# Kernel tuning notes

Hardware: AMD Instinct MI355X
Metric: run time of the kernel (lower is better)

The kernel has to match this reference:

```python
import jax, jax.numpy as jnp
import numpy as np

D = 4096
N_HEAD = 32
KV_HEAD = 8
GS = D * KV_HEAD // N_HEAD  # 1024, kv projection width
B, S = 1, 2048


def setup_inputs() -> dict:
    key = jax.random.key(0)
    ks = jax.random.split(key, 10)
    sc = 0.02
    return {
        "x": jax.random.normal(ks[0], (B, S, D), dtype=jnp.float32),
        "y": jax.random.normal(ks[1], (B, S, D), dtype=jnp.float32),
        "Wq": jax.random.normal(ks[2], (D, D), dtype=jnp.float32) * sc,
        "bq": jax.random.normal(ks[3], (D,), dtype=jnp.float32) * sc,
        "Wk": jax.random.normal(ks[4], (D, GS), dtype=jnp.float32) * sc,
        "bk": jax.random.normal(ks[5], (GS,), dtype=jnp.float32) * sc,
        "Wv": jax.random.normal(ks[6], (D, GS), dtype=jnp.float32) * sc,
        "bv": jax.random.normal(ks[7], (GS,), dtype=jnp.float32) * sc,
        "Wo": jax.random.normal(ks[8], (D, D), dtype=jnp.float32) * sc,
        "bo": jax.random.normal(ks[9], (D,), dtype=jnp.float32) * sc,
        "n_head": N_HEAD,
        "kv_head": KV_HEAD,
    }


def reference(x, y, Wq, bq, Wk, bk, Wv, bv, Wo, bo, n_head, kv_head):
    b, s, d = x.shape
    hd = d // n_head              # per-head dim
    gvs = hd // 2                 # complex pairs per head (group_vector_size)
    q = (x @ Wq + bq).reshape(b, s, n_head, hd)
    k = (y @ Wk + bk).reshape(b, s, kv_head, hd)
    v = (y @ Wv + bv).reshape(b, s, kv_head, hd)

    # RoPE: phi = 1/5000**(i/gvs); angle[p, i] = phi[i] * p  (matrix.T in torch)
    phi = 1.0 / (5000.0 ** (jnp.arange(gvs, dtype=jnp.float32) / gvs))
    ang = jnp.arange(s, dtype=jnp.float32)[:, None] * phi[None, :]  # [S, gvs]
    cos = jnp.cos(ang)[None, :, None, :]  # [1,S,1,gvs]
    sin = jnp.sin(ang)[None, :, None, :]

    def rope(t):
        # interleaved pairs (t[...,2i], t[...,2i+1]) form complex numbers
        tr, ti = t[..., 0::2], t[..., 1::2]
        ro = tr * cos - ti * sin
        io = tr * sin + ti * cos
        return jnp.stack([ro, io], axis=-1).reshape(t.shape)

    q = rope(q)
    k = rope(k)

    # GQA: head h uses kv head h // (n_head // kv_head) -> repeat kv heads
    module = n_head // kv_head
    k = jnp.repeat(k, module, axis=2)  # [B,S,H,hd]
    v = jnp.repeat(v, module, axis=2)

    scores = jnp.einsum("bqhd,bkhd->bhqk", q, k) / jnp.sqrt(jnp.float32(hd))
    causal = jnp.tril(jnp.ones((s, s), dtype=bool))
    scores = jnp.where(causal[None, None], scores, -jnp.inf)
    attn = jax.nn.softmax(scores, axis=-1)
    out = jnp.einsum("bhqk,bkhd->bqhd", attn, v).reshape(b, s, d)
    return out @ Wo + bo
```

## Files before the change

kernel.cpp:

```cpp
#include <hip/hip_runtime.h>
#include <hip/hip_bf16.h>

typedef unsigned int uint32;
typedef unsigned short ushort16;
typedef __attribute__((ext_vector_type(8))) __bf16 bf16x8;
typedef __attribute__((ext_vector_type(4))) float f32x4;

__device__ __forceinline__ ushort16 f2bf(float f) {
    uint32 u = __float_as_uint(f);
    u += 0x7fff + ((u >> 16) & 1);
    return (ushort16)(u >> 16);
}
__device__ __forceinline__ uint32 pack2rn(float a, float b) {
    uint32 ua = __float_as_uint(a) + 0x8000u;
    uint32 ub = __float_as_uint(b) + 0x8000u;
    return __builtin_amdgcn_perm(ub, ua, 0x07060302);
}
__device__ __forceinline__ float blo(uint32 u) { return __uint_as_float(u << 16); }
__device__ __forceinline__ float bhi(uint32 u) { return __uint_as_float(u & 0xffff0000u); }

__device__ __forceinline__ void storeC(float v, float* p) { *p = v; }
__device__ __forceinline__ void storeC(float v, ushort16* p) { *p = f2bf(v); }

__device__ __forceinline__ void gload_lds16(const void* g, void* l) {
    __builtin_amdgcn_global_load_lds(
        (const __attribute__((address_space(1))) unsigned int*)g,
        (__attribute__((address_space(3))) unsigned int*)l, 16, 0, 0);
}

#define ROPE_NEGSTEP (-0.19199550593046019f)

__device__ __forceinline__ uint32 rope_pack(float tr, float ti, int ip, int s,
                                            float sc) {
    float inv = exp2f((float)ip * ROPE_NEGSTEP);
    float ang = (float)s * inv;
    float sn = __sinf(ang), cs = __cosf(ang);
    return pack2rn((tr * cs - ti * sn) * sc, (tr * sn + ti * cs) * sc);
}

__global__ __launch_bounds__(256) void prep_kernel(
    const float* __restrict__ x, const float* __restrict__ y,
    const float* __restrict__ Wq, const float* __restrict__ Wk,
    const float* __restrict__ Wv, const float* __restrict__ Wo,
    ushort16* __restrict__ xb, ushort16* __restrict__ yb,
    ushort16* __restrict__ Wqt, ushort16* __restrict__ Wkvt,
    ushort16* __restrict__ Wot)
{
    __shared__ float tile[64][65];
    const int b = blockIdx.x;
    if (b < 8192) {
        const int n8 = 1048576;
        int idx = b * 256 + threadIdx.x;
        const float* S = (idx < n8) ? x : y;
        ushort16*    D = (idx < n8) ? xb : yb;
        int i = (idx < n8) ? idx : idx - n8;
        float4 a = ((const float4*)S)[2 * i];
        float4 c = ((const float4*)S)[2 * i + 1];
        uint4 u;
        u.x = pack2rn(a.x, a.y); u.y = pack2rn(a.z, a.w);
        u.z = pack2rn(c.x, c.y); u.w = pack2rn(c.z, c.w);
        ((uint4*)D)[i] = u;
        return;
    }
    int t = b - 8192;
    int kblk = t & 63, sel = t >> 6;
    const float* W; ushort16* Wt; int N, n0;
    if (sel < 64)      { W = Wq; Wt = Wqt;  N = 4096; n0 = sel * 64; }
    else if (sel < 80) { W = Wk; Wt = Wkvt; N = 1024; n0 = (sel - 64) * 64; }
    else if (sel < 96) { W = Wv; Wt = Wkvt + (size_t)1024 * 4096; N = 1024; n0 = (sel - 80) * 64; }
    else               { W = Wo; Wt = Wot;  N = 4096; n0 = (sel - 96) * 64; }
    const int k0 = kblk * 64;
#pragma unroll
    for (int it = 0; it < 16; ++it) {
        int idx = threadIdx.x + it * 256;
        int r = idx >> 6, c = idx & 63;
        tile[r][c] = W[(size_t)(k0 + r) * N + n0 + c];
    }
    __syncthreads();
#pragma unroll
    for (int it = 0; it < 8; ++it) {
        int idx = threadIdx.x + it * 256;
        int nr = idx >> 5, kp = idx & 31;
        uint32 u = pack2rn(tile[2 * kp][nr], tile[2 * kp + 1][nr]);
        *(uint32*)&Wt[(size_t)(n0 + nr) * 4096 + k0 + 2 * kp] = u;
    }
}

__global__ __launch_bounds__(256) void gemm_qkv(
    const ushort16* __restrict__ xb, const ushort16* __restrict__ yb,
    const ushort16* __restrict__ Wqt, const ushort16* __restrict__ Wkvt,
    const float* __restrict__ bq, const float* __restrict__ bk,
    const float* __restrict__ bv, float* __restrict__ Q,
    ushort16* __restrict__ KVb)
{
    __shared__ __align__(16) ushort16 As[128 * 64];
    __shared__ __align__(16) ushort16 Bs[128 * 64];

    const bool isQ = (blockIdx.x < 32);
    const ushort16* A = isQ ? xb : yb;
    const ushort16* B = isQ ? Wqt : Wkvt;
    const int gn0 = (isQ ? (int)blockIdx.x : (int)blockIdx.x - 32) * 128;
    const int gm0 = blockIdx.y * 128;
    const int K = 4096;

    const int tid  = threadIdx.x;
    const int lane = tid & 63, wave = tid >> 6;
    const int quad = lane >> 4, m16 = lane & 15;
    const int wm = (wave >> 1) * 64, wn = (wave & 1) * 64;

    f32x4 acc[4][4];
#pragma unroll
    for (int i = 0; i < 4; ++i)
#pragma unroll
        for (int j = 0; j < 4; ++j) acc[i][j] = (f32x4){0.f, 0.f, 0.f, 0.f};

    const int rl = lane >> 3, cl = lane & 7;
    const int clog = cl ^ (rl & 7);
    const ushort16* Ag = A + (size_t)(gm0 + wave * 32 + rl) * K + clog * 8;
    const ushort16* Bg = B + (size_t)(gn0 + wave * 32 + rl) * K + clog * 8;
    char* AsW = (char*)As + wave * 4096;
    char* BsW = (char*)Bs + wave * 4096;

    for (int k0 = 0; k0 < K; k0 += 64) {
        __syncthreads();
#pragma unroll
        for (int i = 0; i < 4; ++i) {
            gload_lds16(Ag + (size_t)(8 * i) * K, AsW + i * 1024);
            gload_lds16(Bg + (size_t)(8 * i) * K, BsW + i * 1024);
        }
        Ag += 64; Bg += 64;
        __syncthreads();

#pragma unroll
        for (int s = 0; s < 2; ++s) {
            bf16x8 aF[4], bF[4];
            const int cr = s * 4 + quad;
#pragma unroll
            for (int i = 0; i < 4; ++i) {
                int r = wm + i * 16 + m16;
                aF[i] = *(const bf16x8*)&As[r * 64 + ((cr ^ (r & 7)) * 8)];
                int n = wn + i * 16 + m16;
                bF[i] = *(const bf16x8*)&Bs[n * 64 + ((cr ^ (n & 7)) * 8)];
            }
            __builtin_amdgcn_s_setprio(1);
#pragma unroll
            for (int i = 0; i < 4; ++i)
#pragma unroll
                for (int j = 0; j < 4; ++j)
                    acc[i][j] = __builtin_amdgcn_mfma_f32_16x16x32_bf16(
                        aF[i], bF[j], acc[i][j], 0, 0, 0);
            __builtin_amdgcn_s_setprio(0);
        }
    }

#pragma unroll
    for (int j = 0; j < 4; ++j) {
        int col = gn0 + wn + j * 16 + m16;
        float bb = isQ ? bq[col] : ((col < 1024) ? bk[col] : bv[col - 1024]);
#pragma unroll
        for (int i = 0; i < 4; ++i) {
            int row0 = gm0 + wm + i * 16 + quad * 4;
#pragma unroll
            for (int r = 0; r < 4; ++r) {
                float v = acc[i][j][r] + bb;
                if (isQ) Q[(size_t)(row0 + r) * 4096 + col] = v;
                else     KVb[(size_t)(row0 + r) * 2048 + col] = f2bf(v);
            }
        }
    }
}

template <typename OutT>
__global__ __launch_bounds__(256) void gemm_mfma(
    const ushort16* __restrict__ A, const ushort16* __restrict__ B,
    const float* __restrict__ b1, OutT* __restrict__ C, int N, int K)
{
    __shared__ __align__(16) ushort16 As[128 * 64];
    __shared__ __align__(16) ushort16 Bs[128 * 64];

    const int tid  = threadIdx.x;
    const int lane = tid & 63, wave = tid >> 6;
    const int quad = lane >> 4, m16 = lane & 15;
    const int wm = (wave >> 1) * 64, wn = (wave & 1) * 64;
    const int gm0 = blockIdx.y * 128, gn0 = blockIdx.x * 128;

    f32x4 acc[4][4];
#pragma unroll
    for (int i = 0; i < 4; ++i)
#pragma unroll
        for (int j = 0; j < 4; ++j) acc[i][j] = (f32x4){0.f, 0.f, 0.f, 0.f};

    const int rl = lane >> 3, cl = lane & 7;
    const int clog = cl ^ (rl & 7);
    const ushort16* Ag = A + (size_t)(gm0 + wave * 32 + rl) * K + clog * 8;
    const ushort16* Bg = B + (size_t)(gn0 + wave * 32 + rl) * K + clog * 8;
    char* AsW = (char*)As + wave * 4096;
    char* BsW = (char*)Bs + wave * 4096;

    for (int k0 = 0; k0 < K; k0 += 64) {
        __syncthreads();
#pragma unroll
        for (int i = 0; i < 4; ++i) {
            gload_lds16(Ag + (size_t)(8 * i) * K, AsW + i * 1024);
            gload_lds16(Bg + (size_t)(8 * i) * K, BsW + i * 1024);
        }
        Ag += 64; Bg += 64;
        __syncthreads();

#pragma unroll
        for (int s = 0; s < 2; ++s) {
            bf16x8 aF[4], bF[4];
            const int cr = s * 4 + quad;
#pragma unroll
            for (int i = 0; i < 4; ++i) {
                int r = wm + i * 16 + m16;
                aF[i] = *(const bf16x8*)&As[r * 64 + ((cr ^ (r & 7)) * 8)];
                int n = wn + i * 16 + m16;
                bF[i] = *(const bf16x8*)&Bs[n * 64 + ((cr ^ (n & 7)) * 8)];
            }
            __builtin_amdgcn_s_setprio(1);
#pragma unroll
            for (int i = 0; i < 4; ++i)
#pragma unroll
                for (int j = 0; j < 4; ++j)
                    acc[i][j] = __builtin_amdgcn_mfma_f32_16x16x32_bf16(
                        aF[i], bF[j], acc[i][j], 0, 0, 0);
            __builtin_amdgcn_s_setprio(0);
        }
    }

#pragma unroll
    for (int j = 0; j < 4; ++j) {
        int col = gn0 + wn + j * 16 + m16;
        float bb = b1[col];
#pragma unroll
        for (int i = 0; i < 4; ++i) {
            int row0 = gm0 + wm + i * 16 + quad * 4;
#pragma unroll
            for (int r = 0; r < 4; ++r)
                storeC(acc[i][j][r] + bb, C + (size_t)(row0 + r) * N + col);
        }
    }
}

__global__ __launch_bounds__(256) void ropek_vt_kernel(
    ushort16* __restrict__ KVb, ushort16* __restrict__ Vt)
{
    __shared__ ushort16 tile[64][66];
    const int b = blockIdx.x;
    if (b < 4096) {
        int idx = b * 256 + threadIdx.x;
        int i   = idx & 63;
        int rem = idx >> 6;
        int s   = rem >> 3, h = rem & 7;
        float inv = exp2f((float)i * ROPE_NEGSTEP);
        float ang = (float)s * inv;
        float cs = __cosf(ang), sn = __sinf(ang);
        uint32* p = (uint32*)&KVb[(size_t)s * 2048 + h * 128 + 2 * i];
        uint32 u = *p;
        float tr = blo(u), ti = bhi(u);
        *p = pack2rn(tr * cs - ti * sn, tr * sn + ti * cs);
        return;
    }
    int t = b - 4096;
    int s0 = (t >> 4) * 64, d0 = (t & 15) * 64;
#pragma unroll
    for (int it = 0; it < 2; ++it) {
        int i = threadIdx.x + it * 256;
        int r = i >> 3, c = (i & 7) * 8;
        *(uint4*)&tile[r][c] = *(const uint4*)&KVb[(size_t)(s0 + r) * 2048 + 1024 + d0 + c];
    }
    __syncthreads();
#pragma unroll
    for (int it = 0; it < 2; ++it) {
        int i = threadIdx.x + it * 256;
        int dr = i >> 3, sc = (i & 7) * 8;
        uint32 w[4];
#pragma unroll
        for (int q = 0; q < 4; ++q)
            w[q] = (uint32)tile[sc + 2 * q][dr] | ((uint32)tile[sc + 2 * q + 1][dr] << 16);
        *(uint4*)&Vt[(size_t)(d0 + dr) * 2048 + s0 + sc] = *(uint4*)w;
    }
}

__global__ __launch_bounds__(256) void flash_attn_kernel(
    const float* __restrict__ Qf, const ushort16* __restrict__ KVb,
    const ushort16* __restrict__ Vtg, ushort16* __restrict__ O)
{
    __shared__ __align__(16) ushort16 Kb[2][64 * 128];
    __shared__ __align__(16) ushort16 Vs[128 * 64];
    __shared__ __align__(16) ushort16 Ps[64 * 72];

    const int tid  = threadIdx.x;
    const int lane = tid & 63, wave = tid >> 6;
    const int quad = lane >> 4, m16 = lane & 15;
    const int h = (int)blockIdx.y, kvh = h >> 2;

    const ushort16* Kbase = KVb + kvh * 128;
    const ushort16* Vbase = Vtg + (size_t)(kvh * 128) * 2048;

    const int rK = lane >> 4;
    const ushort16* pKe = Kbase + (size_t)(wave * 16 + rK) * 2048
                        + (((lane & 15) ^ rK) * 8);
    const ushort16* pKo = Kbase + (size_t)(wave * 16 + 4 + rK) * 2048
                        + (((lane & 15) ^ (4 + rK)) * 8);
    const int rV = lane >> 3;
    const ushort16* pV  = Vbase + (size_t)(wave * 32 + rV) * 2048
                        + (((lane & 7) ^ rV) * 8);
    char* ldsK0 = (char*)&Kb[0][0] + wave * 4096;
    char* ldsK1 = (char*)&Kb[1][0] + wave * 4096;
    char* ldsV  = (char*)&Vs[0]    + wave * 4096;

#define STAGE_K(dst, kk) do {                                   \
        const ushort16* _s0 = pKe + (size_t)(kk) * 2048;        \
        const ushort16* _s1 = pKo + (size_t)(kk) * 2048;        \
        gload_lds16(_s0,            (dst));                     \
        gload_lds16(_s1,            (dst) + 1024);              \
        gload_lds16(_s0 + 8 * 2048, (dst) + 2048);              \
        gload_lds16(_s1 + 8 * 2048, (dst) + 3072);              \
    } while (0)
#define STAGE_V(kk) do {                                        \
        const ushort16* _sv = pV + (kk);                        \
        gload_lds16(_sv,             ldsV);                     \
        gload_lds16(_sv +  8 * 2048, ldsV + 1024);              \
        gload_lds16(_sv + 16 * 2048, ldsV + 2048);              \
        gload_lds16(_sv + 24 * 2048, ldsV + 3072);              \
    } while (0)

    for (int pass = 0; pass < 2; ++pass) {
        const int qi = pass ? (int)blockIdx.x : 31 - (int)blockIdx.x;
        const int q0 = qi * 64;
        const int srow = q0 + wave * 16 + m16;

        const float sc = 0.08838834764831845f * 1.4426950408889634f;
        bf16x8 qa[4];
        {
            const float* qp = Qf + (size_t)srow * 4096 + h * 128 + quad * 8;
#pragma unroll
            for (int ks = 0; ks < 4; ++ks) {
                float4 a = *(const float4*)(qp + ks * 32);
                float4 b = *(const float4*)(qp + ks * 32 + 4);
                int ip0 = quad * 4 + ks * 16;
                uint4 u;
                u.x = rope_pack(a.x, a.y, ip0 + 0, srow, sc);
                u.y = rope_pack(a.z, a.w, ip0 + 1, srow, sc);
                u.z = rope_pack(b.x, b.y, ip0 + 2, srow, sc);
                u.w = rope_pack(b.z, b.w, ip0 + 3, srow, sc);
                qa[ks] = *(bf16x8*)&u;
            }
        }

        f32x4 acc_o[8];
#pragma unroll
        for (int t = 0; t < 8; ++t) acc_o[t] = (f32x4){0.f, 0.f, 0.f, 0.f};
        float m_i[4], l_i[4];
#pragma unroll
        for (int r = 0; r < 4; ++r) { m_i[r] = -1e30f; l_i[r] = 0.f; }

        int cur = 0;
        STAGE_K(ldsK0, 0);

        for (int k0 = 0; k0 <= q0; k0 += 64) {
            __syncthreads();

            STAGE_V(k0);
            const bool pre = (k0 + 64 <= q0);
            if (pre) STAGE_K(cur ? ldsK0 : ldsK1, k0 + 64);

            const ushort16* Kcur = &Kb[cur][0];

            f32x4 sacc[4];
#pragma unroll
            for (int j = 0; j < 4; ++j) sacc[j] = (f32x4){0.f, 0.f, 0.f, 0.f};
            __builtin_amdgcn_s_setprio(1);
#pragma unroll
            for (int ks = 0; ks < 4; ++ks) {
#pragma unroll
                for (int j = 0; j < 4; ++j) {
                    int n = j * 16 + m16;
                    bf16x8 kb = *(const bf16x8*)&Kcur[n * 128 + (((ks * 4 + quad) ^ (n & 7)) * 8)];
                    sacc[j] = __builtin_amdgcn_mfma_f32_16x16x32_bf16(qa[ks], kb, sacc[j], 0, 0, 0);
                }
            }
            __builtin_amdgcn_s_setprio(0);

            if (k0 == q0) {
                int qr = wave * 16 + quad * 4;
#pragma unroll
                for (int j = 0; j < 4; ++j) {
                    int kvl = j * 16 + m16;
#pragma unroll
                    for (int r = 0; r < 4; ++r)
                        if (kvl > qr + r) sacc[j][r] = -1e30f;
                }
            }

            float rm[4];
#pragma unroll
            for (int r = 0; r < 4; ++r) {
                float v = fmaxf(fmaxf(sacc[0][r], sacc[1][r]), fmaxf(sacc[2][r], sacc[3][r]));
                v = fmaxf(v, __shfl_xor(v, 1));
                v = fmaxf(v, __shfl_xor(v, 2));
                v = fmaxf(v, __shfl_xor(v, 4));
                v = fmaxf(v, __shfl_xor(v, 8));
                rm[r] = v;
            }
            int ok = (rm[0] <= m_i[0]) & (rm[1] <= m_i[1]) &
                     (rm[2] <= m_i[2]) & (rm[3] <= m_i[3]);
            if (!__all(ok)) {
#pragma unroll
                for (int r = 0; r < 4; ++r) {
                    float mnew = fmaxf(m_i[r], rm[r]);
                    float al = exp2f(m_i[r] - mnew);
                    l_i[r] *= al;
                    m_i[r] = mnew;
#pragma unroll
                    for (int t = 0; t < 8; ++t) acc_o[t][r] *= al;
                }
            }
#pragma unroll
            for (int r = 0; r < 4; ++r) {
                float rs = 0.f;
#pragma unroll
                for (int j = 0; j < 4; ++j) {
                    float pv = exp2f(sacc[j][r] - m_i[r]);
                    sacc[j][r] = pv;
                    rs += pv;
                }
                rs += __shfl_xor(rs, 1);
                rs += __shfl_xor(rs, 2);
                rs += __shfl_xor(rs, 4);
                rs += __shfl_xor(rs, 8);
                l_i[r] += rs;
                int q = wave * 16 + quad * 4 + r;
#pragma unroll
                for (int j = 0; j < 4; ++j) {
                    int kv = j * 16 + m16;
                    Ps[q * 72 + (((kv >> 3) ^ (q & 7)) * 8) + (kv & 7)] = f2bf(sacc[j][r]);
                }
            }

            if (pre) { asm volatile("s_waitcnt vmcnt(4)" ::: "memory"); }
            else     { asm volatile("s_waitcnt vmcnt(0)" ::: "memory"); }
            __builtin_amdgcn_sched_barrier(0);
            __builtin_amdgcn_s_barrier();

            int qrow = wave * 16 + m16;
#pragma unroll
            for (int ks2 = 0; ks2 < 2; ++ks2) {
                bf16x8 pa = *(const bf16x8*)&Ps[qrow * 72 + (((ks2 * 4 + quad) ^ (qrow & 7)) * 8)];
                __builtin_amdgcn_s_setprio(1);
#pragma unroll
                for (int t = 0; t < 8; ++t) {
                    int d = t * 16 + m16;
                    bf16x8 vb = *(const bf16x8*)&Vs[d * 64 + (((ks2 * 4 + quad) ^ (d & 7)) * 8)];
                    acc_o[t] = __builtin_amdgcn_mfma_f32_16x16x32_bf16(pa, vb, acc_o[t], 0, 0, 0);
                }
                __builtin_amdgcn_s_setprio(0);
            }
            cur ^= 1;
        }

        ushort16* op = O + (size_t)(q0 + wave * 16 + quad * 4) * 4096 + h * 128 + m16;
#pragma unroll
        for (int r = 0; r < 4; ++r) {
            float inv = 1.0f / l_i[r];
#pragma unroll
            for (int t = 0; t < 8; ++t)
                op[(size_t)r * 4096 + t * 16] = f2bf(acc_o[t][r] * inv);
        }
    }
#undef STAGE_K
#undef STAGE_V
}

extern "C" void kernel_launch(void* const* d_in, const int* in_sizes, int n_in,
                              void* d_out, int out_size, void* d_ws, size_t ws_size,
                              hipStream_t stream)
{
    const float* x  = (const float*)d_in[0];
    const float* y  = (const float*)d_in[1];
    const float* Wq = (const float*)d_in[2];
    const float* bq = (const float*)d_in[3];
    const float* Wk = (const float*)d_in[4];
    const float* bk = (const float*)d_in[5];
    const float* Wv = (const float*)d_in[6];
    const float* bv = (const float*)d_in[7];
    const float* Wo = (const float*)d_in[8];
    const float* bo = (const float*)d_in[9];
    float* out = (float*)d_out;

    const size_t MB = 1024 * 1024;

    char* ws = (char*)d_ws;
    ushort16* xb   = (ushort16*)(ws);
    ushort16* yb   = (ushort16*)(ws + 16 * MB);
    ushort16* Wqt  = (ushort16*)(ws + 32 * MB);
    ushort16* Wkvt = (ushort16*)(ws + 64 * MB);
    ushort16* Wot  = (ushort16*)(ws + 80 * MB);
    ushort16* KVb  = (ushort16*)(ws + 112 * MB);
    ushort16* Vtg  = (ushort16*)(ws + 120 * MB);
    ushort16* Ao   = yb;
    float*    Q    = out;

    prep_kernel<<<18432, 256, 0, stream>>>(x, y, Wq, Wk, Wv, Wo,
                                           xb, yb, Wqt, Wkvt, Wot);

    gemm_qkv<<<dim3(48, 16), 256, 0, stream>>>(
        xb, yb, Wqt, Wkvt, bq, bk, bv, Q, KVb);

    ropek_vt_kernel<<<4608, 256, 0, stream>>>(KVb, Vtg);

    flash_attn_kernel<<<dim3(16, 32), 256, 0, stream>>>(Q, KVb, Vtg, Ao);

    gemm_mfma<float><<<dim3(32, 16), 256, 0, stream>>>(
        Ao, Wot, bo, out, 4096, 4096);
}
```

Before: 567.9 us.

## Process both causal query tiles in one KV sweep and use DPP row reductions

```diff
diff --git a/kernel.cpp b/kernel.cpp
--- a/kernel.cpp
+++ b/kernel.cpp
@@ -26,6 +26,25 @@
     __builtin_amdgcn_global_load_lds(
         (const __attribute__((address_space(1))) unsigned int*)g,
         (__attribute__((address_space(3))) unsigned int*)l, 16, 0, 0);
+}
+
+#define DPP_ROR(v, n)                                                        \
+    __uint_as_float(__builtin_amdgcn_update_dpp(                             \
+        (int)__float_as_uint(v), (int)__float_as_uint(v), 0x120 + (n),       \
+        0xf, 0xf, false))
+__device__ __forceinline__ float rowmax16(float v) {
+    v = fmaxf(v, DPP_ROR(v, 8));
+    v = fmaxf(v, DPP_ROR(v, 4));
+    v = fmaxf(v, DPP_ROR(v, 2));
+    v = fmaxf(v, DPP_ROR(v, 1));
+    return v;
+}
+__device__ __forceinline__ float rowsum16(float v) {
+    v += DPP_ROR(v, 8);
+    v += DPP_ROR(v, 4);
+    v += DPP_ROR(v, 2);
+    v += DPP_ROR(v, 1);
+    return v;
 }
 
 #define ROPE_NEGSTEP (-0.19199550593046019f)
@@ -289,7 +308,7 @@
 {
     __shared__ __align__(16) ushort16 Kb[2][64 * 128];
     __shared__ __align__(16) ushort16 Vs[128 * 64];
-    __shared__ __align__(16) ushort16 Ps[64 * 72];
+    __shared__ __align__(16) ushort16 Ps[2][64 * 72];
 
     const int tid  = threadIdx.x;
     const int lane = tid & 63, wave = tid >> 6;
@@ -327,95 +346,119 @@
         gload_lds16(_sv + 24 * 2048, ldsV + 3072);              \
     } while (0)
 
-    for (int pass = 0; pass < 2; ++pass) {
-        const int qi = pass ? (int)blockIdx.x : 31 - (int)blockIdx.x;
-        const int q0 = qi * 64;
-        const int srow = q0 + wave * 16 + m16;
-
-        const float sc = 0.08838834764831845f * 1.4426950408889634f;
-        bf16x8 qa[4];
+    const int q0A = (31 - (int)blockIdx.x) * 64;
+    const int q0B = (int)blockIdx.x * 64;
+    const float sc = 0.08838834764831845f * 1.4426950408889634f;
+
+    bf16x8 qaA[4], qaB[4];
+    {
+        const int rowA = q0A + wave * 16 + m16;
+        const int rowB = q0B + wave * 16 + m16;
+        const float* qpA = Qf + (size_t)rowA * 4096 + h * 128 + quad * 8;
+        const float* qpB = Qf + (size_t)rowB * 4096 + h * 128 + quad * 8;
+#pragma unroll
+        for (int ks = 0; ks < 4; ++ks) {
+            int ip0 = quad * 4 + ks * 16;
+            float4 a = *(const float4*)(qpA + ks * 32);
+            float4 b = *(const float4*)(qpA + ks * 32 + 4);
+            uint4 u;
+            u.x = rope_pack(a.x, a.y, ip0 + 0, rowA, sc);
+            u.y = rope_pack(a.z, a.w, ip0 + 1, rowA, sc);
+            u.z = rope_pack(b.x, b.y, ip0 + 2, rowA, sc);
+            u.w = rope_pack(b.z, b.w, ip0 + 3, rowA, sc);
+            qaA[ks] = *(bf16x8*)&u;
+            a = *(const float4*)(qpB + ks * 32);
+            b = *(const float4*)(qpB + ks * 32 + 4);
+            u.x = rope_pack(a.x, a.y, ip0 + 0, rowB, sc);
+            u.y = rope_pack(a.z, a.w, ip0 + 1, rowB, sc);
+            u.z = rope_pack(b.x, b.y, ip0 + 2, rowB, sc);
+            u.w = rope_pack(b.z, b.w, ip0 + 3, rowB, sc);
+            qaB[ks] = *(bf16x8*)&u;
+        }
+    }
+
+    f32x4 accA[8], accB[8];
+#pragma unroll
+    for (int t = 0; t < 8; ++t) {
+        accA[t] = (f32x4){0.f, 0.f, 0.f, 0.f};
+        accB[t] = (f32x4){0.f, 0.f, 0.f, 0.f};
+    }
+    float mA[4], lA[4], mB[4], lB[4];
+#pragma unroll
+    for (int r = 0; r < 4; ++r) {
+        mA[r] = -1e30f; lA[r] = 0.f; mB[r] = -1e30f; lB[r] = 0.f;
+    }
+
+    int cur = 0;
+    STAGE_K(ldsK0, 0);
+
+    for (int k0 = 0; k0 <= q0A; k0 += 64) {
+        __syncthreads();
+
+        STAGE_V(k0);
+        const bool pre = (k0 + 64 <= q0A);
+        if (pre) STAGE_K(cur ? ldsK0 : ldsK1, k0 + 64);
+        const bool doB = (k0 <= q0B);
+
+        const ushort16* Kcur = &Kb[cur][0];
+
+        f32x4 sA[4], sB[4];
+#pragma unroll
+        for (int j = 0; j < 4; ++j) {
+            sA[j] = (f32x4){0.f, 0.f, 0.f, 0.f};
+            sB[j] = (f32x4){0.f, 0.f, 0.f, 0.f};
+        }
+        __builtin_amdgcn_s_setprio(1);
+#pragma unroll
+        for (int ks = 0; ks < 4; ++ks) {
+#pragma unroll
+            for (int j = 0; j < 4; ++j) {
+                int n = j * 16 + m16;
+                bf16x8 kb = *(const bf16x8*)&Kcur[n * 128 + (((ks * 4 + quad) ^ (n & 7)) * 8)];
+                sA[j] = __builtin_amdgcn_mfma_f32_16x16x32_bf16(qaA[ks], kb, sA[j], 0, 0, 0);
+                if (doB)
+                    sB[j] = __builtin_amdgcn_mfma_f32_16x16x32_bf16(qaB[ks], kb, sB[j], 0, 0, 0);
+            }
+        }
+        __builtin_amdgcn_s_setprio(0);
+
+        if (k0 == q0A) {
+            int qr = wave * 16 + quad * 4;
+#pragma unroll
+            for (int j = 0; j < 4; ++j) {
+                int kvl = j * 16 + m16;
+#pragma unroll
+                for (int r = 0; r < 4; ++r)
+                    if (kvl > qr + r) sA[j][r] = -1e30f;
+            }
+        }
+        if (k0 == q0B) {
+            int qr = wave * 16 + quad * 4;
+#pragma unroll
+            for (int j = 0; j < 4; ++j) {
+                int kvl = j * 16 + m16;
+#pragma unroll
+                for (int r = 0; r < 4; ++r)
+                    if (kvl > qr + r) sB[j][r] = -1e30f;
+            }
+        }
+
         {
-            const float* qp = Qf + (size_t)srow * 4096 + h * 128 + quad * 8;
-#pragma unroll
-            for (int ks = 0; ks < 4; ++ks) {
-                float4 a = *(const float4*)(qp + ks * 32);
-                float4 b = *(const float4*)(qp + ks * 32 + 4);
-                int ip0 = quad * 4 + ks * 16;
-                uint4 u;
-                u.x = rope_pack(a.x, a.y, ip0 + 0, srow, sc);
-                u.y = rope_pack(a.z, a.w, ip0 + 1, srow, sc);
-                u.z = rope_pack(b.x, b.y, ip0 + 2, srow, sc);
-                u.w = rope_pack(b.z, b.w, ip0 + 3, srow, sc);
-                qa[ks] = *(bf16x8*)&u;
-            }
-        }
-
-        f32x4 acc_o[8];
-#pragma unroll
-        for (int t = 0; t < 8; ++t) acc_o[t] = (f32x4){0.f, 0.f, 0.f, 0.f};
-        float m_i[4], l_i[4];
-#pragma unroll
-        for (int r = 0; r < 4; ++r) { m_i[r] = -1e30f; l_i[r] = 0.f; }
-
-        int cur = 0;
-        STAGE_K(ldsK0, 0);
-
-        for (int k0 = 0; k0 <= q0; k0 += 64) {
-            __syncthreads();
-
-            STAGE_V(k0);
-            const bool pre = (k0 + 64 <= q0);
-            if (pre) STAGE_K(cur ? ldsK0 : ldsK1, k0 + 64);
-
-            const ushort16* Kcur = &Kb[cur][0];
-
-            f32x4 sacc[4];
-#pragma unroll
-            for (int j = 0; j < 4; ++j) sacc[j] = (f32x4){0.f, 0.f, 0.f, 0.f};
-            __builtin_amdgcn_s_setprio(1);
-#pragma unroll
-            for (int ks = 0; ks < 4; ++ks) {
-#pragma unroll
-                for (int j = 0; j < 4; ++j) {
-                    int n = j * 16 + m16;
-                    bf16x8 kb = *(const bf16x8*)&Kcur[n * 128 + (((ks * 4 + quad) ^ (n & 7)) * 8)];
-                    sacc[j] = __builtin_amdgcn_mfma_f32_16x16x32_bf16(qa[ks], kb, sacc[j], 0, 0, 0);
-                }
-            }
-            __builtin_amdgcn_s_setprio(0);
-
-            if (k0 == q0) {
-                int qr = wave * 16 + quad * 4;
-#pragma unroll
-                for (int j = 0; j < 4; ++j) {
-                    int kvl = j * 16 + m16;
-#pragma unroll
-                    for (int r = 0; r < 4; ++r)
-                        if (kvl > qr + r) sacc[j][r] = -1e30f;
-                }
-            }
-
             float rm[4];
 #pragma unroll
-            for (int r = 0; r < 4; ++r) {
-                float v = fmaxf(fmaxf(sacc[0][r], sacc[1][r]), fmaxf(sacc[2][r], sacc[3][r]));
-                v = fmaxf(v, __shfl_xor(v, 1));
-                v = fmaxf(v, __shfl_xor(v, 2));
-                v = fmaxf(v, __shfl_xor(v, 4));
-                v = fmaxf(v, __shfl_xor(v, 8));
-                rm[r] = v;
-            }
-            int ok = (rm[0] <= m_i[0]) & (rm[1] <= m_i[1]) &
-                     (rm[2] <= m_i[2]) & (rm[3] <= m_i[3]);
+            for (int r = 0; r < 4; ++r)
+                rm[r] = rowmax16(fmaxf(fmaxf(sA[0][r], sA[1][r]),
+                                       fmaxf(sA[2][r], sA[3][r])));
+            int ok = (rm[0] <= mA[0]) & (rm[1] <= mA[1]) &
+                     (rm[2] <= mA[2]) & (rm[3] <= mA[3]);
             if (!__all(ok)) {
 #pragma unroll
                 for (int r = 0; r < 4; ++r) {
-                    float mnew = fmaxf(m_i[r], rm[r]);
-                    float al = exp2f(m_i[r] - mnew);
-                    l_i[r] *= al;
-                    m_i[r] = mnew;
-#pragma unroll
-                    for (int t = 0; t < 8; ++t) acc_o[t][r] *= al;
+                    float mnew = fmaxf(mA[r], rm[r]);
+                    float al = exp2f(mA[r] - mnew);
+                    lA[r] *= al; mA[r] = mnew;
+#pragma unroll
+                    for (int t = 0; t < 8; ++t) accA[t][r] *= al;
                 }
             }
 #pragma unroll
@@ -423,51 +466,96 @@
                 float rs = 0.f;
 #pragma unroll
                 for (int j = 0; j < 4; ++j) {
-                    float pv = exp2f(sacc[j][r] - m_i[r]);
-                    sacc[j][r] = pv;
-                    rs += pv;
+                    float pv = exp2f(sA[j][r] - mA[r]);
+                    sA[j][r] = pv; rs += pv;
                 }
-                rs += __shfl_xor(rs, 1);
-                rs += __shfl_xor(rs, 2);
-                rs += __shfl_xor(rs, 4);
-                rs += __shfl_xor(rs, 8);
-                l_i[r] += rs;
+                lA[r] += rowsum16(rs);
                 int q = wave * 16 + quad * 4 + r;
 #pragma unroll
                 for (int j = 0; j < 4; ++j) {
                     int kv = j * 16 + m16;
-                    Ps[q * 72 + (((kv >> 3) ^ (q & 7)) * 8) + (kv & 7)] = f2bf(sacc[j][r]);
+                    Ps[0][q * 72 + (((kv >> 3) ^ (q & 7)) * 8) + (kv & 7)] = f2bf(sA[j][r]);
                 }
             }
-
-            if (pre) { asm volatile("s_waitcnt vmcnt(4)" ::: "memory"); }
-            else     { asm volatile("s_waitcnt vmcnt(0)" ::: "memory"); }
-            __builtin_amdgcn_sched_barrier(0);
-            __builtin_amdgcn_s_barrier();
-
-            int qrow = wave * 16 + m16;
-#pragma unroll
-            for (int ks2 = 0; ks2 < 2; ++ks2) {
-                bf16x8 pa = *(const bf16x8*)&Ps[qrow * 72 + (((ks2 * 4 + quad) ^ (qrow & 7)) * 8)];
-                __builtin_amdgcn_s_setprio(1);
-#pragma unroll
-                for (int t = 0; t < 8; ++t) {
-                    int d = t * 16 + m16;
-                    bf16x8 vb = *(const bf16x8*)&Vs[d * 64 + (((ks2 * 4 + quad) ^ (d & 7)) * 8)];
-                    acc_o[t] = __builtin_amdgcn_mfma_f32_16x16x32_bf16(pa, vb, acc_o[t], 0, 0, 0);
+        }
+        if (doB) {
+            float rm[4];
+#pragma unroll
+            for (int r = 0; r < 4; ++r)
+                rm[r] = rowmax16(fmaxf(fmaxf(sB[0][r], sB[1][r]),
+                                       fmaxf(sB[2][r], sB[3][r])));
+            int ok = (rm[0] <= mB[0]) & (rm[1] <= mB[1]) &
+                     (rm[2] <= mB[2]) & (rm[3] <= mB[3]);
+            if (!__all(ok)) {
+#pragma unroll
+                for (int r = 0; r < 4; ++r) {
+                    float mnew = fmaxf(mB[r], rm[r]);
+                    float al = exp2f(mB[r] - mnew);
+                    lB[r] *= al; mB[r] = mnew;
+#pragma unroll
+                    for (int t = 0; t < 8; ++t) accB[t][r] *= al;
                 }
-                __builtin_amdgcn_s_setprio(0);
-            }
-            cur ^= 1;
-        }
-
-        ushort16* op = O + (size_t)(q0 + wave * 16 + quad * 4) * 4096 + h * 128 + m16;
+            }
+#pragma unroll
+            for (int r = 0; r < 4; ++r) {
+                float rs = 0.f;
+#pragma unroll
+                for (int j = 0; j < 4; ++j) {
+                    float pv = exp2f(sB[j][r] - mB[r]);
+                    sB[j][r] = pv; rs += pv;
+                }
+                lB[r] += rowsum16(rs);
+                int q = wave * 16 + quad * 4 + r;
+#pragma unroll
+                for (int j = 0; j < 4; ++j) {
+                    int kv = j * 16 + m16;
+                    Ps[1][q * 72 + (((kv >> 3) ^ (q & 7)) * 8) + (kv & 7)] = f2bf(sB[j][r]);
+                }
+            }
+        }
+
+        if (pre) { asm volatile("s_waitcnt vmcnt(4)" ::: "memory"); }
+        else     { asm volatile("s_waitcnt vmcnt(0)" ::: "memory"); }
+        __builtin_amdgcn_sched_barrier(0);
+        __builtin_amdgcn_s_barrier();
+
+        int qrow = wave * 16 + m16;
+#pragma unroll
+        for (int ks2 = 0; ks2 < 2; ++ks2) {
+            bf16x8 paA = *(const bf16x8*)&Ps[0][qrow * 72 + (((ks2 * 4 + quad) ^ (qrow & 7)) * 8)];
+            bf16x8 paB;
+            if (doB)
+                paB = *(const bf16x8*)&Ps[1][qrow * 72 + (((ks2 * 4 + quad) ^ (qrow & 7)) * 8)];
+            __builtin_amdgcn_s_setprio(1);
+#pragma unroll
+            for (int t = 0; t < 8; ++t) {
+                int d = t * 16 + m16;
+                bf16x8 vb = *(const bf16x8*)&Vs[d * 64 + (((ks2 * 4 + quad) ^ (d & 7)) * 8)];
+                accA[t] = __builtin_amdgcn_mfma_f32_16x16x32_bf16(paA, vb, accA[t], 0, 0, 0);
+                if (doB)
+                    accB[t] = __builtin_amdgcn_mfma_f32_16x16x32_bf16(paB, vb, accB[t], 0, 0, 0);
+            }
+            __builtin_amdgcn_s_setprio(0);
+        }
+        cur ^= 1;
+    }
+
+    {
+        ushort16* op = O + (size_t)(q0A + wave * 16 + quad * 4) * 4096 + h * 128 + m16;
 #pragma unroll
         for (int r = 0; r < 4; ++r) {
-            float inv = 1.0f / l_i[r];
+            float inv = 1.0f / lA[r];
 #pragma unroll
             for (int t = 0; t < 8; ++t)
-                op[(size_t)r * 4096 + t * 16] = f2bf(acc_o[t][r] * inv);
+                op[(size_t)r * 4096 + t * 16] = f2bf(accA[t][r] * inv);
+        }
+        op = O + (size_t)(q0B + wave * 16 + quad * 4) * 4096 + h * 128 + m16;
+#pragma unroll
+        for (int r = 0; r < 4; ++r) {
+            float inv = 1.0f / lB[r];
+#pragma unroll
+            for (int t = 0; t < 8; ++t)
+                op[(size_t)r * 4096 + t * 16] = f2bf(accB[t][r] * inv);
         }
     }
 #undef STAGE_K
```

After: 722.5 us. 27.2% more time.
